# Kernel optimization log

Measured on AMD Instinct MI355X. Metric: run time of the kernel, lower is better.

Reference implementation:

```python
import jax, jax.numpy as jnp
import numpy as np

HEADS = 32
HID = 4096
HD = HID // HEADS          # head_dim = 128
ROT = HD // 2              # rotary dim per stream = 64
SEQ = 2048


def _rope(x, pos):
    # x: [S, H, ROT]; pos: [S] int. GPT-NeoX-style interleaved pair rotation.
    d = x.shape[-1]
    inv_freq = 1.0 / (10000.0 ** (jnp.arange(0, d, 2, dtype=jnp.float32) / d))  # [d/2]
    ang = pos.astype(jnp.float32)[:, None] * inv_freq[None, :]                   # [S, d/2]
    cos = jnp.cos(ang)[:, None, :]
    sin = jnp.sin(ang)[:, None, :]
    xp = x.reshape(x.shape[0], x.shape[1], d // 2, 2)
    xe, xo = xp[..., 0], xp[..., 1]
    return jnp.stack([xe * cos - xo * sin, xe * sin + xo * cos], axis=-1).reshape(x.shape)


def setup_inputs() -> dict:
    key = jax.random.key(0)
    ks = jax.random.split(key, 6)
    return {
        "hidden_states": jax.random.normal(ks[0], (SEQ, HID), dtype=jnp.float32),
        "position_ids": jax.random.randint(ks[1], (2, SEQ), 0, SEQ),
        "W_qkv": jax.random.normal(ks[2], (HID, 3 * HID), dtype=jnp.float32) * 0.02,
        "b_qkv": jnp.zeros((3 * HID,), dtype=jnp.float32),
        "W_dense": jax.random.normal(ks[3], (HID, HID), dtype=jnp.float32) * 0.02,
        "b_dense": jnp.zeros((HID,), dtype=jnp.float32),
    }


def reference(hidden_states, position_ids, W_qkv, b_qkv, W_dense, b_dense):
    S = hidden_states.shape[0]
    # fused QKV projection; per-head packed layout [head][q|k|v]
    qkv = (hidden_states @ W_qkv + b_qkv).reshape(S, HEADS, 3, HD)
    q, k, v = qkv[:, :, 0], qkv[:, :, 1], qkv[:, :, 2]      # each [S, H, HD]
    p = position_ids[0] + 1
    b = position_ids[1] + 1
    def rot2(t):
        # 2D RoPE: first half rotated by position stream p, second by b
        return jnp.concatenate([_rope(t[..., :ROT], p), _rope(t[..., ROT:], b)], axis=-1)
    q = rot2(q)
    k = rot2(k)
    scale = 1.0 / jnp.sqrt(jnp.float32(HD))
    scores = jnp.einsum('shd,thd->hst', q, k) * scale        # [H, S, S]
    causal = jnp.tril(jnp.ones((S, S), dtype=bool))
    scores = jnp.where(causal[None], scores, jnp.float32(-1e9))
    attn = jax.nn.softmax(scores, axis=-1)
    ctx = jnp.einsum('hst,thd->shd', attn, v).reshape(S, HID)
    return ctx @ W_dense + b_dense
```

## Files before the change

kernel.cpp:

```cpp
#include <hip/hip_runtime.h>
#include <cstdint>
#include <cstdio>

typedef unsigned short u16;
typedef short bf16x8 __attribute__((ext_vector_type(8)));
typedef float f32x4 __attribute__((ext_vector_type(4)));
typedef unsigned short u16x8 __attribute__((ext_vector_type(8)));

#define SEQL 2048
#define NHEADS 32
#define HDIM 128
#define HIDDEN 4096

__device__ __forceinline__ u16 f2bf(float x){
  union { float f; unsigned u; } v; v.f = x;
  unsigned r = v.u + 0x7fffu + ((v.u >> 16) & 1u);
  return (u16)(r >> 16);
}
__device__ __forceinline__ float bf2f(u16 x){
  union { unsigned u; float f; } v; v.u = ((unsigned)x) << 16;
  return v.f;
}
__device__ __forceinline__ float exp2_asm(float x){
  float r; asm("v_exp_f32 %0, %1" : "=v"(r) : "v"(x)); return r;
}
__device__ __forceinline__ unsigned cvtpk_bf16(float lo, float hi){
  unsigned r; asm("v_cvt_pk_bf16_f32 %0, %1, %2" : "=v"(r) : "v"(lo), "v"(hi)); return r;
}

__device__ __forceinline__ void gload_lds16(const u16* g, u16* l){
  __builtin_amdgcn_global_load_lds((const __attribute__((address_space(1))) void*)g,
                                   (__attribute__((address_space(3))) void*)l, 16, 0, 0);
}

__global__ void cast_hs_kernel(const float* __restrict__ in, u16* __restrict__ out, int n8){
  int i = blockIdx.x * blockDim.x + threadIdx.x;
  if (i >= n8) return;
  const float4* p = (const float4*)in + (size_t)i*2;
  float4 a = p[0], b = p[1];
  u16x8 o;
  o[0]=f2bf(a.x); o[1]=f2bf(a.y); o[2]=f2bf(a.z); o[3]=f2bf(a.w);
  o[4]=f2bf(b.x); o[5]=f2bf(b.y); o[6]=f2bf(b.z); o[7]=f2bf(b.w);
  *((u16x8*)out + i) = o;
}

__global__ void wtrans_kernel(const float* __restrict__ W, u16* __restrict__ Wt,
                              int Ntot, int n0, int K){
  __shared__ float t[32][33];
  int tx = threadIdx.x, ty = threadIdx.y;
  int nn = blockIdx.x*32, k0 = blockIdx.y*32;
  #pragma unroll
  for (int i=0;i<4;i++)
    t[ty*4+i][tx] = W[(size_t)(k0+ty*4+i)*Ntot + n0 + nn + tx];
  __syncthreads();
  #pragma unroll
  for (int i=0;i<4;i++)
    Wt[(size_t)(nn+ty*4+i)*K + k0 + tx] = f2bf(t[tx][ty*4+i]);
}

template<int OUT_BF16>
__global__ __launch_bounds__(512, 2) void gemm8_kernel(const u16* __restrict__ A, const u16* __restrict__ Bt,
                              const float* __restrict__ bias, void* __restrict__ Cv,
                              int K, int ldC)
{
  extern __shared__ u16 lds[];
  int tid = threadIdx.x;
  int lane = tid & 63;
  int wave = tid >> 6;
  int lr = lane & 15, lg = lane >> 4;
  int wm = wave >> 2, wn = wave & 3;

  int nwg = gridDim.x;
  int cpx = nwg >> 3;
  int b0 = blockIdx.x;
  int swz = (b0 & 7) * cpx + (b0 >> 3);
  int bm = swz & 7, bn = swz >> 3;
  int m0 = bm * 256, n0 = bn * 256;
  int NT = K >> 6;

  int r0 = tid >> 3;
  int cb0 = ((tid & 7) ^ (r0 & 7)) * 8;

  const u16* A0p = A  + (size_t)m0*K;
  const u16* A1p = A  + (size_t)(m0+128)*K;
  const u16* B0p = Bt + (size_t)n0*K;
  const u16* B1p = Bt + (size_t)(n0+128)*K;

  #define STAGE8(G, SLOT) do {                                        \
    gload_lds16((G) + (size_t)r0*K + cb0, lds + (SLOT) + tid*8);      \
    gload_lds16((G) + (size_t)(r0+64)*K + cb0, lds + (SLOT) + (tid+512)*8); \
  } while(0)

  int x7 = lr & 7;
  int colk0 = (lg ^ x7)*8;
  int colk1 = ((4 + lg) ^ x7)*8;
  int rA[4], rB[2];
  #pragma unroll
  for (int f=0; f<4; f++) rA[f] = (wm*64 + f*16 + lr)*64;
  #pragma unroll
  for (int nf=0; nf<2; nf++) rB[nf] = (wn*32 + nf*16 + lr)*64;

  f32x4 acc[8][4] = {};
  bf16x8 a_[4][2], b0r[2][2], b1r[2][2];

  STAGE8(A0p,      0);
  STAGE8(B0p,   8192);
  STAGE8(B1p,  16384);
  STAGE8(A1p,  24576);
  STAGE8(A0p + 64, 32768);
  STAGE8(B0p + 64, 40960);
  STAGE8(B1p + 64, 49152);
  asm volatile("s_waitcnt vmcnt(6)" ::: "memory");
  asm volatile("s_barrier" ::: "memory");

  for (int T = 0; T < NT; ++T){
    int d = (T & 1) << 15;
    int e = d ^ 32768;
    const u16* sA0 = lds + d;
    const u16* sB0 = lds + d + 8192;
    const u16* sB1 = lds + d + 16384;
    const u16* sA1 = lds + d + 24576;
    int kc  = (T+1) << 6;
    int kc2 = (T+2) << 6;
    bool st2 = (T+2) < NT;

    #pragma unroll
    for (int f=0; f<4; f++){
      a_[f][0] = *(const bf16x8*)&sA0[rA[f] + colk0];
      a_[f][1] = *(const bf16x8*)&sA0[rA[f] + colk1];
    }
    #pragma unroll
    for (int nf=0; nf<2; nf++){
      b0r[nf][0] = *(const bf16x8*)&sB0[rB[nf] + colk0];
      b0r[nf][1] = *(const bf16x8*)&sB0[rB[nf] + colk1];
    }
    if (T+1 < NT) STAGE8(A1p + kc, e + 24576);
    asm volatile("s_barrier" ::: "memory");
    asm volatile("s_waitcnt lgkmcnt(0)" ::: "memory");
    __builtin_amdgcn_sched_barrier(0);
    __builtin_amdgcn_s_setprio(1);
    #pragma unroll
    for (int f=0; f<4; f++){
      #pragma unroll
      for (int nf=0; nf<2; nf++){
        acc[f][nf] = __builtin_amdgcn_mfma_f32_16x16x32_bf16(a_[f][0], b0r[nf][0], acc[f][nf], 0, 0, 0);
        acc[f][nf] = __builtin_amdgcn_mfma_f32_16x16x32_bf16(a_[f][1], b0r[nf][1], acc[f][nf], 0, 0, 0);
      }
    }
    __builtin_amdgcn_s_setprio(0);
    asm volatile("s_barrier" ::: "memory");

    #pragma unroll
    for (int nf=0; nf<2; nf++){
      b1r[nf][0] = *(const bf16x8*)&sB1[rB[nf] + colk0];
      b1r[nf][1] = *(const bf16x8*)&sB1[rB[nf] + colk1];
    }
    if (st2) STAGE8(A0p + kc2, d);
    asm volatile("s_barrier" ::: "memory");
    asm volatile("s_waitcnt lgkmcnt(0)" ::: "memory");
    __builtin_amdgcn_sched_barrier(0);
    __builtin_amdgcn_s_setprio(1);
    #pragma unroll
    for (int f=0; f<4; f++){
      #pragma unroll
      for (int nf=0; nf<2; nf++){
        acc[f][2+nf] = __builtin_amdgcn_mfma_f32_16x16x32_bf16(a_[f][0], b1r[nf][0], acc[f][2+nf], 0, 0, 0);
        acc[f][2+nf] = __builtin_amdgcn_mfma_f32_16x16x32_bf16(a_[f][1], b1r[nf][1], acc[f][2+nf], 0, 0, 0);
      }
    }
    __builtin_amdgcn_s_setprio(0);
    asm volatile("s_barrier" ::: "memory");

    #pragma unroll
    for (int f=0; f<4; f++){
      a_[f][0] = *(const bf16x8*)&sA1[rA[f] + colk0];
      a_[f][1] = *(const bf16x8*)&sA1[rA[f] + colk1];
    }
    if (st2) STAGE8(B0p + kc2, d + 8192);
    asm volatile("s_barrier" ::: "memory");
    asm volatile("s_waitcnt lgkmcnt(0)" ::: "memory");
    __builtin_amdgcn_sched_barrier(0);
    __builtin_amdgcn_s_setprio(1);
    #pragma unroll
    for (int f=0; f<4; f++){
      #pragma unroll
      for (int nf=0; nf<2; nf++){
        acc[4+f][2+nf] = __builtin_amdgcn_mfma_f32_16x16x32_bf16(a_[f][0], b1r[nf][0], acc[4+f][2+nf], 0, 0, 0);
        acc[4+f][2+nf] = __builtin_amdgcn_mfma_f32_16x16x32_bf16(a_[f][1], b1r[nf][1], acc[4+f][2+nf], 0, 0, 0);
      }
    }
    __builtin_amdgcn_s_setprio(0);
    asm volatile("s_barrier" ::: "memory");

    if (st2) STAGE8(B1p + kc2, d + 16384);
    __builtin_amdgcn_s_setprio(1);
    #pragma unroll
    for (int f=0; f<4; f++){
      #pragma unroll
      for (int nf=0; nf<2; nf++){
        acc[4+f][nf] = __builtin_amdgcn_mfma_f32_16x16x32_bf16(a_[f][0], b0r[nf][0], acc[4+f][nf], 0, 0, 0);
        acc[4+f][nf] = __builtin_amdgcn_mfma_f32_16x16x32_bf16(a_[f][1], b0r[nf][1], acc[4+f][nf], 0, 0, 0);
      }
    }
    __builtin_amdgcn_s_setprio(0);
    if (T+1 < NT){
      if (st2) asm volatile("s_waitcnt vmcnt(6)" ::: "memory");
      else     asm volatile("s_waitcnt vmcnt(0)" ::: "memory");
    }
    asm volatile("s_barrier" ::: "memory");
  }
  #undef STAGE8

  #pragma unroll
  for (int mh=0; mh<2; mh++){
    #pragma unroll
    for (int f=0; f<4; f++){
      #pragma unroll
      for (int nh=0; nh<2; nh++){
        #pragma unroll
        for (int nf=0; nf<2; nf++){
          #pragma unroll
          for (int jj=0; jj<4; jj++){
            int gr = m0 + mh*128 + wm*64 + f*16 + lg*4 + jj;
            int gc = n0 + nh*128 + wn*32 + nf*16 + lr;
            float v = acc[mh*4+f][nh*2+nf][jj] + bias[gc];
            if (OUT_BF16) ((u16*)Cv)[(size_t)gr*ldC + gc] = f2bf(v);
            else          ((float*)Cv)[(size_t)gr*ldC + gc] = v;
          }
        }
      }
    }
  }
}

template<int OUT_BF16>
__global__ __launch_bounds__(512) void gemm3_kernel(const u16* __restrict__ A, const u16* __restrict__ Bt,
                              const float* __restrict__ bias, void* __restrict__ Cv,
                              int K, int ldC, int NBM)
{
  extern __shared__ u16 lds[];
  int tid = threadIdx.x;
  int lane = tid & 63;
  int wave = tid >> 6;
  int lr = lane & 15, lg = lane >> 4;
  int wm = wave >> 2, wn = wave & 3;

  int nwg = gridDim.x;
  int cpx = nwg >> 3;
  int b0 = blockIdx.x;
  int swz = (b0 & 7) * cpx + (b0 >> 3);
  int bm = swz % NBM, bn = swz / NBM;
  int m0 = bm * 128, n0 = bn * 256;

  int NT = K >> 6;

  unsigned offA[2]; int ldsA[2];
  #pragma unroll
  for (int i=0;i<2;i++){
    int c = tid + i*512;
    int row = c >> 3, blk = c & 7;
    offA[i] = (unsigned)(m0 + row)*K + (unsigned)((blk ^ (row & 7))*8);
    ldsA[i] = c*8;
  }
  unsigned offB[4]; int ldsB[4];
  #pragma unroll
  for (int i=0;i<4;i++){
    int c = tid + i*512;
    int row = c >> 3, blk = c & 7;
    offB[i] = (unsigned)(n0 + row)*K + (unsigned)((blk ^ (row & 7))*8);
    ldsB[i] = c*8;
  }

  int colk[2];
  colk[0] = ((lg)     ^ (lr & 7))*8;
  colk[1] = ((4 + lg) ^ (lr & 7))*8;
  int rA[4], rB[4];
  #pragma unroll
  for (int m=0;m<4;m++) rA[m] = (wm*64 + m*16 + lr)*64;
  #pragma unroll
  for (int n=0;n<4;n++) rB[n] = (wn*64 + n*16 + lr)*64;

  f32x4 acc[4][4] = {};

  #pragma unroll
  for (int tt=0; tt<2; ++tt){
    u16* dA = lds + tt*24576;
    u16* dB = dA + 8192;
    int k0 = tt*64;
    #pragma unroll
    for (int i=0;i<2;i++) gload_lds16(A + offA[i] + k0, dA + ldsA[i]);
    #pragma unroll
    for (int i=0;i<4;i++) gload_lds16(Bt + offB[i] + k0, dB + ldsB[i]);
  }
  asm volatile("s_waitcnt vmcnt(6)" ::: "memory");
  asm volatile("s_barrier" ::: "memory");

  int p = 0, s2 = 2;
  for (int t = 0; t < NT; ++t){
    const u16* bA = lds + p*24576;
    const u16* bB = bA + 8192;
    u16* dA = lds + s2*24576;
    u16* dB = dA + 8192;
    bool st = (t + 2) < NT;
    int k2 = (t + 2) << 6;

    bf16x8 a_[4][2], bf0[2][2];
    #pragma unroll
    for (int m=0;m<4;m++){
      a_[m][0] = *(const bf16x8*)&bA[rA[m] + colk[0]];
      a_[m][1] = *(const bf16x8*)&bA[rA[m] + colk[1]];
    }
    #pragma unroll
    for (int n=0;n<2;n++){
      bf0[n][0] = *(const bf16x8*)&bB[rB[n] + colk[0]];
      bf0[n][1] = *(const bf16x8*)&bB[rB[n] + colk[1]];
    }
    if (st){
      gload_lds16(A + offA[0] + k2, dA + ldsA[0]);
      gload_lds16(A + offA[1] + k2, dA + ldsA[1]);
      gload_lds16(Bt + offB[0] + k2, dB + ldsB[0]);
    }
    asm volatile("s_barrier" ::: "memory");
    asm volatile("s_waitcnt lgkmcnt(0)" ::: "memory");
    __builtin_amdgcn_sched_barrier(0);
    __builtin_amdgcn_s_setprio(1);
    #pragma unroll
    for (int m=0;m<4;m++){
      #pragma unroll
      for (int n=0;n<2;n++){
        acc[m][n] = __builtin_amdgcn_mfma_f32_16x16x32_bf16(a_[m][0], bf0[n][0], acc[m][n], 0, 0, 0);
        acc[m][n] = __builtin_amdgcn_mfma_f32_16x16x32_bf16(a_[m][1], bf0[n][1], acc[m][n], 0, 0, 0);
      }
    }
    __builtin_amdgcn_s_setprio(0);
    asm volatile("s_barrier" ::: "memory");

    bf16x8 bf1[2][2];
    #pragma unroll
    for (int n=0;n<2;n++){
      bf1[n][0] = *(const bf16x8*)&bB[rB[n+2] + colk[0]];
      bf1[n][1] = *(const bf16x8*)&bB[rB[n+2] + colk[1]];
    }
    if (st){
      gload_lds16(Bt + offB[1] + k2, dB + ldsB[1]);
      gload_lds16(Bt + offB[2] + k2, dB + ldsB[2]);
      gload_lds16(Bt + offB[3] + k2, dB + ldsB[3]);
    }
    asm volatile("s_barrier" ::: "memory");
    asm volatile("s_waitcnt lgkmcnt(0)" ::: "memory");
    __builtin_amdgcn_sched_barrier(0);
    __builtin_amdgcn_s_setprio(1);
    #pragma unroll
    for (int m=0;m<4;m++){
      #pragma unroll
      for (int n=0;n<2;n++){
        acc[m][n+2] = __builtin_amdgcn_mfma_f32_16x16x32_bf16(a_[m][0], bf1[n][0], acc[m][n+2], 0, 0, 0);
        acc[m][n+2] = __builtin_amdgcn_mfma_f32_16x16x32_bf16(a_[m][1], bf1[n][1], acc[m][n+2], 0, 0, 0);
      }
    }
    __builtin_amdgcn_s_setprio(0);
    if (st) asm volatile("s_waitcnt vmcnt(6)" ::: "memory");
    else    asm volatile("s_waitcnt vmcnt(0)" ::: "memory");
    asm volatile("s_barrier" ::: "memory");

    p = (p == 2) ? 0 : p + 1;
    s2 = (s2 == 2) ? 0 : s2 + 1;
  }

  #pragma unroll
  for (int m=0;m<4;m++){
    #pragma unroll
    for (int n=0;n<4;n++){
      #pragma unroll
      for (int j=0;j<4;j++){
        int gr = m0 + wm*64 + m*16 + lg*4 + j;
        int gc = n0 + wn*64 + n*16 + lr;
        float v = acc[m][n][j] + bias[gc];
        if (OUT_BF16) ((u16*)Cv)[(size_t)gr*ldC + gc] = f2bf(v);
        else          ((float*)Cv)[(size_t)gr*ldC + gc] = v;
      }
    }
  }
}

__global__ __launch_bounds__(256) void rope_kernel(const u16* __restrict__ qkv, const int* __restrict__ pos,
                            u16* __restrict__ Q, u16* __restrict__ Kc, u16* __restrict__ V)
{
  int s = blockIdx.x*4 + (threadIdx.x >> 6);
  int h = blockIdx.y;
  int i = threadIdx.x & 63;
  int half = i >> 5, ii = i & 31;
  int d0 = half*64 + ii*2;
  const u16* base = qkv + (size_t)s*12288 + h*384;
  unsigned qp = *(const unsigned*)&base[d0];
  unsigned kp = *(const unsigned*)&base[128 + d0];
  unsigned vp = *(const unsigned*)&base[256 + d0];
  float qe = bf2f((u16)qp), qo = bf2f((u16)(qp >> 16));
  float ke = bf2f((u16)kp), ko = bf2f((u16)(kp >> 16));
  float pv = (float)(pos[half*SEQL + s] + 1);
  float fr = exp2f(-(float)ii * 0.4152410118609203f);
  float ang = pv * fr;
  float sn, cs; sincosf(ang, &sn, &cs);
  const float sc = 0.1275174313f;
  float q0 = (qe*cs - qo*sn)*sc, q1 = (qe*sn + qo*cs)*sc;
  float k0 = ke*cs - ko*sn,      k1 = ke*sn + ko*cs;
  size_t ob = ((size_t)h*SEQL + s)*HDIM + d0;
  *(unsigned*)&Q[ob]  = (unsigned)f2bf(q0) | ((unsigned)f2bf(q1) << 16);
  *(unsigned*)&Kc[ob] = (unsigned)f2bf(k0) | ((unsigned)f2bf(k1) << 16);
  *(unsigned*)&V[ob]  = vp;
}

__global__ void vtrans_kernel(const u16* __restrict__ V, u16* __restrict__ Vt){
  __shared__ u16 t[32][33];
  int h = blockIdx.z;
  int d0 = blockIdx.x*32, s0 = blockIdx.y*32;
  int tx = threadIdx.x, ty = threadIdx.y;
  const u16* Vh = V + (size_t)h*SEQL*HDIM;
  u16* Vth = Vt + (size_t)h*HDIM*SEQL;
  #pragma unroll
  for (int i=0;i<4;i++)
    t[ty*4+i][tx] = Vh[(size_t)(s0+ty*4+i)*HDIM + d0 + tx];
  __syncthreads();
  #pragma unroll
  for (int i=0;i<4;i++)
    Vth[(size_t)(d0+ty*4+i)*SEQL + s0 + tx] = t[tx][ty*4+i];
}

__global__ __launch_bounds__(256) void attn_kernel(const u16* __restrict__ Q, const u16* __restrict__ Kc,
                             const u16* __restrict__ Vt, u16* __restrict__ ctx)
{
  __shared__ u16 lK[2][64*128];
  __shared__ u16 lV[2][128*64];
  __shared__ u16 P[4*16*68];
  int qt = (gridDim.x - 1) - blockIdx.x;
  int h = blockIdx.y;
  int tid = threadIdx.x;
  int lane = tid & 63;
  int wave = tid >> 6;
  int lr = lane & 15, lg = lane >> 4;
  int q0a = qt*128 + wave*16;
  int q0b = q0a + 64;
  int qa = q0a + lr, qb = q0b + lr;
  const u16* Qh = Q  + (size_t)h*SEQL*HDIM;
  const u16* Kh = Kc + (size_t)h*SEQL*HDIM;
  const u16* Vh = Vt + (size_t)h*HDIM*SEQL;
  u16* Pw = &P[wave*1088];

  bf16x8 qfa[4], qfb[4];
  #pragma unroll
  for (int k32=0;k32<4;k32++){
    qfa[k32] = *(const bf16x8*)&Qh[(size_t)(q0a+lr)*HDIM + k32*32 + lg*8];
    qfb[k32] = *(const bf16x8*)&Qh[(size_t)(q0b+lr)*HDIM + k32*32 + lg*8];
  }

  f32x4 oa[8] = {}, ob[8] = {};
  float ma = -1e30f, la = 0.f;
  float mb = -1e30f, lb = 0.f;

  int nt = (qt+1)*2;

  #define STAGE64(BUF, T0) do {                                             \
    _Pragma("unroll")                                                       \
    for (int i=0;i<4;i++){                                                  \
      int c = i*256 + tid;                                                  \
      int row = c >> 4, b = c & 15;                                         \
      int bp = b ^ (row & 7);                                               \
      gload_lds16(Kh + (size_t)((T0) + row)*HDIM + bp*8, &lK[BUF][c*8]);    \
    }                                                                       \
    _Pragma("unroll")                                                       \
    for (int i=0;i<4;i++){                                                  \
      int c = i*256 + tid;                                                  \
      int dd = c >> 3, b = c & 7;                                           \
      int bp = b ^ (dd & 7);                                                \
      gload_lds16(Vh + (size_t)dd*SEQL + (T0) + bp*8, &lV[BUF][c*8]);       \
    }                                                                       \
  } while(0)

  #define SMAX(S4, O, MRUN, LRUN, QROW, Q0S, PA0, PA1) do {                 \
    float sv[16];                                                           \
    _Pragma("unroll")                                                       \
    for (int g=0;g<4;g++){                                                  \
      _Pragma("unroll")                                                     \
      for (int j=0;j<4;j++) sv[g*4+j] = S4[g][j];                           \
    }                                                                       \
    if (t0 + 63 > (Q0S)){             \
      int kb = t0 + lg*4;                                                   \
      _Pragma("unroll")                                                     \
      for (int g=0;g<4;g++){                                                \
        _Pragma("unroll")                                                   \
        for (int j=0;j<4;j++)                                               \
          sv[g*4+j] = (kb + g*16 + j > (QROW)) ? -1e30f : sv[g*4+j];        \
      }                                                                     \
    }                                                                       \
    float mx = fmaxf(                                                       \
      fmaxf(fmaxf(fmaxf(sv[0],sv[1]),fmaxf(sv[2],sv[3])),                   \
            fmaxf(fmaxf(sv[4],sv[5]),fmaxf(sv[6],sv[7]))),                  \
      fmaxf(fmaxf(fmaxf(sv[8],sv[9]),fmaxf(sv[10],sv[11])),                 \
            fmaxf(fmaxf(sv[12],sv[13]),fmaxf(sv[14],sv[15]))));             \
    mx = fmaxf(mx, __shfl_xor(mx, 16));                                     \
    mx = fmaxf(mx, __shfl_xor(mx, 32));                                     \
    if (!__all(mx <= (MRUN) + 11.5415603f)){                                \
      float mnew = fmaxf((MRUN), mx);                                       \
      float scl = exp2_asm((MRUN) - mnew);                                  \
      (LRUN) *= scl;                                                        \
      (MRUN) = mnew;                                                        \
      float sj[4];                                                          \
      _Pragma("unroll")                                                     \
      for (int j=0;j<4;j++) sj[j] = __shfl(scl, lg*4 + j);                  \
      _Pragma("unroll")                                                     \
      for (int n=0;n<8;n++){                                                \
        _Pragma("unroll")                                                   \
        for (int j=0;j<4;j++) O[n][j] *= sj[j];                             \
      }                                                                     \
    }                                                                       \
    float pr[16];                                                           \
    _Pragma("unroll")                                                       \
    for (int i=0;i<16;i++) pr[i] = exp2_asm(sv[i] - (MRUN));                \
    float sm = (((pr[0]+pr[1]) + (pr[2]+pr[3])) + ((pr[4]+pr[5]) + (pr[6]+pr[7]))) \
             + (((pr[8]+pr[9]) + (pr[10]+pr[11])) + ((pr[12]+pr[13]) + (pr[14]+pr[15]))); \
    sm += __shfl_xor(sm, 16);                                               \
    sm += __shfl_xor(sm, 32);                                               \
    (LRUN) += sm;                                                           \
    _Pragma("unroll")                                                       \
    for (int g=0;g<4;g++){                                                  \
      uint2 w;                                                              \
      w.x = cvtpk_bf16(pr[g*4],   pr[g*4+1]);                               \
      w.y = cvtpk_bf16(pr[g*4+2], pr[g*4+3]);                               \
      *(uint2*)&Pw[lr*68 + g*16 + lg*4] = w;                                \
    }                                                                       \
    PA0 = *(const bf16x8*)&Pw[lr*68 + lg*8];                                \
    PA1 = *(const bf16x8*)&Pw[lr*68 + 32 + lg*8];                           \
  } while(0)

  STAGE64(0, 0);
  __syncthreads();

  for (int t = 0; t < nt; ++t){
    int t0 = t*64;
    int cur = t & 1;
    if (t+1 < nt) STAGE64(cur^1, t0+64);

    const u16* Kt  = &lK[cur][0];
    const u16* Vtl = &lV[cur][0];
    bool ba = (t0 <= q0a + 15);

    f32x4 s4a[4] = {}, s4b[4] = {};
    if (ba){
      #pragma unroll
      for (int g=0; g<4; g++){
        int r = g*16 + lr;
        #pragma unroll
        for (int k32=0;k32<4;k32++){
          bf16x8 kf = *(const bf16x8*)&Kt[r*128 + ((((k32<<2)|lg) ^ (lr&7)))*8];
          s4a[g] = __builtin_amdgcn_mfma_f32_16x16x32_bf16(kf, qfa[k32], s4a[g], 0, 0, 0);
          s4b[g] = __builtin_amdgcn_mfma_f32_16x16x32_bf16(kf, qfb[k32], s4b[g], 0, 0, 0);
        }
      }
    } else {
      #pragma unroll
      for (int g=0; g<4; g++){
        int r = g*16 + lr;
        #pragma unroll
        for (int k32=0;k32<4;k32++){
          bf16x8 kf = *(const bf16x8*)&Kt[r*128 + ((((k32<<2)|lg) ^ (lr&7)))*8];
          s4b[g] = __builtin_amdgcn_mfma_f32_16x16x32_bf16(kf, qfb[k32], s4b[g], 0, 0, 0);
        }
      }
    }

    bf16x8 paa0, paa1, pab0, pab1;
    if (ba) SMAX(s4a, oa, ma, la, qa, q0a, paa0, paa1);
    SMAX(s4b, ob, mb, lb, qb, q0b, pab0, pab1);

    if (ba){
      #pragma unroll
      for (int n=0;n<8;n++){
        int dd = n*16 + lr;
        bf16x8 v0 = *(const bf16x8*)&Vtl[dd*64 + ((lg ^ (dd&7)))*8];
        bf16x8 v1 = *(const bf16x8*)&Vtl[dd*64 + (((4|lg) ^ (dd&7)))*8];
        oa[n] = __builtin_amdgcn_mfma_f32_16x16x32_bf16(paa0, v0, oa[n], 0, 0, 0);
        oa[n] = __builtin_amdgcn_mfma_f32_16x16x32_bf16(paa1, v1, oa[n], 0, 0, 0);
        ob[n] = __builtin_amdgcn_mfma_f32_16x16x32_bf16(pab0, v0, ob[n], 0, 0, 0);
        ob[n] = __builtin_amdgcn_mfma_f32_16x16x32_bf16(pab1, v1, ob[n], 0, 0, 0);
      }
    } else {
      #pragma unroll
      for (int n=0;n<8;n++){
        int dd = n*16 + lr;
        bf16x8 v0 = *(const bf16x8*)&Vtl[dd*64 + ((lg ^ (dd&7)))*8];
        bf16x8 v1 = *(const bf16x8*)&Vtl[dd*64 + (((4|lg) ^ (dd&7)))*8];
        ob[n] = __builtin_amdgcn_mfma_f32_16x16x32_bf16(pab0, v0, ob[n], 0, 0, 0);
        ob[n] = __builtin_amdgcn_mfma_f32_16x16x32_bf16(pab1, v1, ob[n], 0, 0, 0);
      }
    }
    __syncthreads();
  }
  #undef SMAX
  #undef STAGE64

  #pragma unroll
  for (int j=0;j<4;j++){
    float lja = __shfl(la, lg*4 + j);
    float inva = 1.f / lja;
    int srowa = q0a + lg*4 + j;
    #pragma unroll
    for (int n=0;n<8;n++)
      ctx[(size_t)srowa*HIDDEN + h*HDIM + n*16 + lr] = f2bf(oa[n][j]*inva);
    float ljb = __shfl(lb, lg*4 + j);
    float invb = 1.f / ljb;
    int srowb = q0b + lg*4 + j;
    #pragma unroll
    for (int n=0;n<8;n++)
      ctx[(size_t)srowb*HIDDEN + h*HDIM + n*16 + lr] = f2bf(ob[n][j]*invb);
  }
}

extern "C" void kernel_launch(void* const* d_in, const int* in_sizes, int n_in,
                              void* d_out, int out_size, void* d_ws, size_t ws_size,
                              hipStream_t stream)
{
  const float* hs   = (const float*)d_in[0];
  const int*   pos  = (const int*)d_in[1];
  const float* Wqkv = (const float*)d_in[2];
  const float* bqkv = (const float*)d_in[3];
  const float* Wd   = (const float*)d_in[4];
  const float* bd   = (const float*)d_in[5];

  const size_t o_hs  = 0;
  const size_t o_qkv = 16777216;
  const size_t o_Wtq = 67108864;
  const size_t o_Q   = 67108864;
  const size_t o_K   = 83886080;
  const size_t o_V   = 100663296;
  const size_t o_Vt  = 117440512;
  const size_t o_Wtd = 134217728;
  const size_t need  = 167772160;
  if (ws_size < need){
    fprintf(stderr, "kernel_launch: ws too small: %zu < %zu\n", ws_size, need);
    return;
  }
  char* w = (char*)d_ws;
  u16* hsb = (u16*)(w + o_hs);
  u16* qkv = (u16*)(w + o_qkv);
  u16* ctx = (u16*)(w + o_qkv);
  u16* Wtq = (u16*)(w + o_Wtq);
  u16* Qs  = (u16*)(w + o_Q);
  u16* Ks  = (u16*)(w + o_K);
  u16* Vs  = (u16*)(w + o_V);
  u16* Vts = (u16*)(w + o_Vt);
  u16* Wtd = (u16*)(w + o_Wtd);

  const size_t g8_lds = 65536*sizeof(u16);
  const size_t g3_lds = 3*24576*sizeof(u16);

  cast_hs_kernel<<<dim3(4096), dim3(256), 0, stream>>>(hs, hsb, SEQL*HIDDEN/8);
  wtrans_kernel<<<dim3(384,128), dim3(32,8), 0, stream>>>(Wqkv, Wtq, 12288, 0, 4096);

  gemm8_kernel<1><<<dim3(8*32), dim3(512), g8_lds, stream>>>(
      hsb, Wtq, bqkv, (void*)qkv, HIDDEN, 12288);
  gemm3_kernel<1><<<dim3(16*16), dim3(512), g3_lds, stream>>>(
      hsb, Wtq + (size_t)8192*HIDDEN, bqkv + 8192, (void*)(qkv + 8192),
      HIDDEN, 12288, 16);

  wtrans_kernel<<<dim3(128,128), dim3(32,8), 0, stream>>>(Wd, Wtd, 4096, 0, 4096);

  rope_kernel<<<dim3(SEQL/4, NHEADS), dim3(256), 0, stream>>>(qkv, pos, Qs, Ks, Vs);
  vtrans_kernel<<<dim3(4, 64, NHEADS), dim3(32,8), 0, stream>>>(Vs, Vts);
  attn_kernel<<<dim3(SEQL/128, NHEADS), dim3(256), 0, stream>>>(Qs, Ks, Vts, ctx);

  gemm3_kernel<0><<<dim3(16*16), dim3(512), g3_lds, stream>>>(
      ctx, Wtd, bd, d_out, HIDDEN, HIDDEN, 16);
}
```

Before: 484.5 us.

## Read K and V fragments directly from global memory in attention kernel

```diff
diff --git a/kernel.cpp b/kernel.cpp
--- a/kernel.cpp
+++ b/kernel.cpp
@@ -429,8 +429,6 @@
 __global__ __launch_bounds__(256) void attn_kernel(const u16* __restrict__ Q, const u16* __restrict__ Kc,
                              const u16* __restrict__ Vt, u16* __restrict__ ctx)
 {
-  __shared__ u16 lK[2][64*128];
-  __shared__ u16 lV[2][128*64];
   __shared__ u16 P[4*16*68];
   int qt = (gridDim.x - 1) - blockIdx.x;
   int h = blockIdx.y;
@@ -458,23 +456,6 @@
   float mb = -1e30f, lb = 0.f;
 
   int nt = (qt+1)*2;
-
-  #define STAGE64(BUF, T0) do {                                             \
-    _Pragma("unroll")                                                       \
-    for (int i=0;i<4;i++){                                                  \
-      int c = i*256 + tid;                                                  \
-      int row = c >> 4, b = c & 15;                                         \
-      int bp = b ^ (row & 7);                                               \
-      gload_lds16(Kh + (size_t)((T0) + row)*HDIM + bp*8, &lK[BUF][c*8]);    \
-    }                                                                       \
-    _Pragma("unroll")                                                       \
-    for (int i=0;i<4;i++){                                                  \
-      int c = i*256 + tid;                                                  \
-      int dd = c >> 3, b = c & 7;                                           \
-      int bp = b ^ (dd & 7);                                                \
-      gload_lds16(Vh + (size_t)dd*SEQL + (T0) + bp*8, &lV[BUF][c*8]);       \
-    }                                                                       \
-  } while(0)
 
   #define SMAX(S4, O, MRUN, LRUN, QROW, Q0S, PA0, PA1) do {                 \
     float sv[16];                                                           \
@@ -532,16 +513,9 @@
     PA1 = *(const bf16x8*)&Pw[lr*68 + 32 + lg*8];                           \
   } while(0)
 
-  STAGE64(0, 0);
-  __syncthreads();
-
   for (int t = 0; t < nt; ++t){
     int t0 = t*64;
-    int cur = t & 1;
-    if (t+1 < nt) STAGE64(cur^1, t0+64);
-
-    const u16* Kt  = &lK[cur][0];
-    const u16* Vtl = &lV[cur][0];
+    const u16* Kt = Kh + (size_t)t0*HDIM;
     bool ba = (t0 <= q0a + 15);
 
     f32x4 s4a[4] = {}, s4b[4] = {};
@@ -551,7 +525,7 @@
         int r = g*16 + lr;
         #pragma unroll
         for (int k32=0;k32<4;k32++){
-          bf16x8 kf = *(const bf16x8*)&Kt[r*128 + ((((k32<<2)|lg) ^ (lr&7)))*8];
+          bf16x8 kf = *(const bf16x8*)&Kt[(size_t)r*HDIM + (((k32<<2)|lg))*8];
           s4a[g] = __builtin_amdgcn_mfma_f32_16x16x32_bf16(kf, qfa[k32], s4a[g], 0, 0, 0);
           s4b[g] = __builtin_amdgcn_mfma_f32_16x16x32_bf16(kf, qfb[k32], s4b[g], 0, 0, 0);
         }
@@ -562,7 +536,7 @@
         int r = g*16 + lr;
         #pragma unroll
         for (int k32=0;k32<4;k32++){
-          bf16x8 kf = *(const bf16x8*)&Kt[r*128 + ((((k32<<2)|lg) ^ (lr&7)))*8];
+          bf16x8 kf = *(const bf16x8*)&Kt[(size_t)r*HDIM + (((k32<<2)|lg))*8];
           s4b[g] = __builtin_amdgcn_mfma_f32_16x16x32_bf16(kf, qfb[k32], s4b[g], 0, 0, 0);
         }
       }
@@ -576,8 +550,8 @@
       #pragma unroll
       for (int n=0;n<8;n++){
         int dd = n*16 + lr;
-        bf16x8 v0 = *(const bf16x8*)&Vtl[dd*64 + ((lg ^ (dd&7)))*8];
-        bf16x8 v1 = *(const bf16x8*)&Vtl[dd*64 + (((4|lg) ^ (dd&7)))*8];
+        bf16x8 v0 = *(const bf16x8*)&Vh[(size_t)dd*SEQL + t0 + lg*8];
+        bf16x8 v1 = *(const bf16x8*)&Vh[(size_t)dd*SEQL + t0 + 32 + lg*8];
         oa[n] = __builtin_amdgcn_mfma_f32_16x16x32_bf16(paa0, v0, oa[n], 0, 0, 0);
         oa[n] = __builtin_amdgcn_mfma_f32_16x16x32_bf16(paa1, v1, oa[n], 0, 0, 0);
         ob[n] = __builtin_amdgcn_mfma_f32_16x16x32_bf16(pab0, v0, ob[n], 0, 0, 0);
@@ -587,16 +561,14 @@
       #pragma unroll
       for (int n=0;n<8;n++){
         int dd = n*16 + lr;
-        bf16x8 v0 = *(const bf16x8*)&Vtl[dd*64 + ((lg ^ (dd&7)))*8];
-        bf16x8 v1 = *(const bf16x8*)&Vtl[dd*64 + (((4|lg) ^ (dd&7)))*8];
+        bf16x8 v0 = *(const bf16x8*)&Vh[(size_t)dd*SEQL + t0 + lg*8];
+        bf16x8 v1 = *(const bf16x8*)&Vh[(size_t)dd*SEQL + t0 + 32 + lg*8];
         ob[n] = __builtin_amdgcn_mfma_f32_16x16x32_bf16(pab0, v0, ob[n], 0, 0, 0);
         ob[n] = __builtin_amdgcn_mfma_f32_16x16x32_bf16(pab1, v1, ob[n], 0, 0, 0);
       }
     }
-    __syncthreads();
   }
   #undef SMAX
-  #undef STAGE64
 
   #pragma unroll
   for (int j=0;j<4;j++){
```

Result: slower. 606.6 us (+25.2%).
